# Kernel optimization log

Hardware: AMD Instinct MI355X
Metric: run time of the kernel (lower is better)

Reference implementation:

```python
import jax, jax.numpy as jnp
import numpy as np

NEG_SLOPE = 0.2


def setup_inputs() -> dict:
    key = jax.random.key(0)
    ks = jax.random.split(key, 5)
    B, N, QD, KD, H = 32, 16384, 128, 128, 128
    query = jax.random.normal(ks[0], (B, QD), dtype=jnp.float32)
    key_t = jax.random.normal(ks[1], (B, N, KD), dtype=jnp.float32)
    # nn.Linear weights: out = x @ W.T ; scale roughly like torch default init
    Wq = jax.random.normal(ks[2], (H, QD), dtype=jnp.float32) / np.sqrt(QD)
    Wk = jax.random.normal(ks[3], (H, KD), dtype=jnp.float32) / np.sqrt(KD)
    Wa = jax.random.normal(ks[4], (H,), dtype=jnp.float32) / np.sqrt(H)
    return {"query": query, "key": key_t, "Wq": Wq, "Wk": Wk, "Wa": Wa}


def reference(query, key, Wq, Wk, Wa):
    # query: [B, QD], key: [B, N, KD]
    h_query = jnp.einsum('bq,hq->bh', query, Wq)          # [B, H]
    h_key = jnp.einsum('bnk,hk->bnh', key, Wk)            # [B, N, H]
    h = h_query[:, None, :] + h_key                       # broadcast add
    e = jax.nn.leaky_relu(h, negative_slope=NEG_SLOPE)
    e = jnp.einsum('bnh,h->bn', e, Wa)                    # rank-1 attention
    e = jax.nn.softmax(e, axis=-1)                        # [B, N]
    scored = jnp.einsum('bnh,bn->bh', h_key, e)           # weighted sum over nodes
    h_prime = jax.nn.elu(scored)
    return h_prime, e
```

## Files before the change

### kernel.cpp

```cpp
#include <hip/hip_runtime.h>
#include <hip/hip_bf16.h>
#include <math.h>

#define B_ 32
#define N_ 16384
#define D_ 128
#define NEG_SLOPE 0.2f
#define CHUNKS 16
#define ITERS 16

typedef __attribute__((ext_vector_type(8))) short short8;
typedef __attribute__((ext_vector_type(4))) float f32x4;

__device__ __forceinline__ short8 cvt8(float4 x, float4 y) {
    union { unsigned u[4]; short8 s; } r;
    union { __hip_bfloat162 b; unsigned u; } t;
    t.b = __float22bfloat162_rn(make_float2(x.x, x.y)); r.u[0] = t.u;
    t.b = __float22bfloat162_rn(make_float2(x.z, x.w)); r.u[1] = t.u;
    t.b = __float22bfloat162_rn(make_float2(y.x, y.y)); r.u[2] = t.u;
    t.b = __float22bfloat162_rn(make_float2(y.z, y.w)); r.u[3] = t.u;
    return r.s;
}

template<int HALF>
__device__ __forceinline__ void compute_half(const char* lbuf, int ln, int g, int w,
                                             const short8 (&bfrag)[8][4], f32x4 (&acc)[8]) {
    const int r = w * 16 + ln;
    const unsigned swr = (unsigned)(ln & 7) << 4;
#pragma unroll
    for (int kk2 = 0; kk2 < 2; ++kk2) {
        unsigned off0 = (unsigned)(r * 256 + kk2 * 128 + g * 32);
        float4 x = *(const float4*)(lbuf + (off0 ^ swr));
        float4 y = *(const float4*)(lbuf + ((off0 + 16) ^ swr));
        short8 a = cvt8(x, y);
#pragma unroll
        for (int cf = 0; cf < 8; ++cf)
            acc[cf] = __builtin_amdgcn_mfma_f32_16x16x32_bf16(
                a, bfrag[cf][HALF * 2 + kk2], acc[cf], 0, 0, 0);
    }
}

#define WAITV(N) asm volatile("s_waitcnt vmcnt(" #N ")" ::: "memory")

__global__ __launch_bounds__(256, 2) void
main_kernel(const float* __restrict__ query, const float* __restrict__ key,
            const float* __restrict__ Wq, const float* __restrict__ Wk,
            const float* __restrict__ Wa,
            float* __restrict__ logits, float* __restrict__ part) {
    __shared__ float kbuf[4][64 * 64];
    __shared__ float comb_acc[4][D_];
    __shared__ float comb_m[4], comb_l[4];

    const int b = blockIdx.y, chunk = blockIdx.x;
    const int tid = threadIdx.x;
    const int w = tid >> 6;
    const int lane = tid & 63;
    const int ln = lane & 15;
    const int g = lane >> 4;
    const int n0 = chunk * (N_ / CHUNKS);

    short8 bfrag[8][4];
#pragma unroll
    for (int cf = 0; cf < 8; ++cf) {
        const float* wp = Wk + (size_t)(cf * 16 + ln) * D_;
#pragma unroll
        for (int kk = 0; kk < 4; ++kk) {
            const float4* p = (const float4*)(wp + kk * 32 + g * 8);
            bfrag[cf][kk] = cvt8(p[0], p[1]);
        }
    }
    float hq_r[8], wa_r[8];
    {
        const float4* qv = (const float4*)(query + (size_t)b * D_);
#pragma unroll
        for (int cf = 0; cf < 8; ++cf) {
            const float4* wv = (const float4*)(Wq + (size_t)(cf * 16 + ln) * D_ + g * 32);
            float s = 0.f;
#pragma unroll
            for (int u = 0; u < 8; ++u) {
                float4 wq = wv[u], qq = qv[g * 8 + u];
                s = fmaf(wq.x, qq.x, s); s = fmaf(wq.y, qq.y, s);
                s = fmaf(wq.z, qq.z, s); s = fmaf(wq.w, qq.w, s);
            }
            s += __shfl_xor(s, 16);
            s += __shfl_xor(s, 32);
            hq_r[cf] = s;
            wa_r[cf] = Wa[cf * 16 + ln];
        }
    }

    float m_w = -1e30f, l_w = 0.f;
    float accl[8];
#pragma unroll
    for (int cf = 0; cf < 8; ++cf) accl[cf] = 0.f;

    const char* kbase = (const char*)(key + ((size_t)b * N_ + n0) * D_);
    char* lds0 = (char*)&kbuf[0][0];

    auto stage = [&](int s) {
        const int itt = s >> 1, half = s & 1;
        const char* gt = kbase + (size_t)itt * (64 * 512) + half * 256;
        char* lb = lds0 + (s & 3) * 16384 + w * 4096;
        const int rr = lane >> 4;
        const unsigned cb = (unsigned)(lane & 15) * 16;
#pragma unroll
        for (int k = 0; k < 4; ++k) {
            int rowk = k * 4 + rr;
            unsigned src = (unsigned)((w * 16 + rowk) * 512) +
                           (cb ^ (((unsigned)(rowk & 7)) << 4));
            __builtin_amdgcn_global_load_lds(
                (const __attribute__((address_space(1))) unsigned int*)(uintptr_t)(gt + src),
                (__attribute__((address_space(3))) unsigned int*)(uintptr_t)(lb + k * 1024),
                16, 0, 0);
        }
    };

    stage(0); stage(1); stage(2);

    for (int it = 0; it < ITERS; ++it) {
        f32x4 acc[8] = {};
        {
            int s = 2 * it;
            if (s + 3 < 32) stage(s + 3);
            if (it == 0)      WAITV(12);
            else if (it < 15) WAITV(13);
            else              WAITV(6);
            compute_half<0>(lds0 + (s & 3) * 16384, ln, g, w, bfrag, acc);
        }
        {
            int s = 2 * it + 1;
            if (s + 3 < 32) stage(s + 3);
            if (it == 0)       WAITV(12);
            else if (it < 14)  WAITV(13);
            else if (it == 14) WAITV(9);
            else               WAITV(1);
            compute_half<1>(lds0 + (s & 3) * 16384, ln, g, w, bfrag, acc);
        }

        float lg[4];
#pragma unroll
        for (int j = 0; j < 4; ++j) {
            float s = 0.f;
#pragma unroll
            for (int cf = 0; cf < 8; ++cf) {
                float v = hq_r[cf] + acc[cf][j];
                v = (v > 0.f) ? v : (NEG_SLOPE * v);
                s = fmaf(v, wa_r[cf], s);
            }
            s += __shfl_xor(s, 1);
            s += __shfl_xor(s, 2);
            s += __shfl_xor(s, 4);
            s += __shfl_xor(s, 8);
            lg[j] = s;
        }
        int nbase = n0 + it * 64 + w * 16;
        if (ln == 0)
            *(float4*)&logits[(size_t)b * N_ + nbase + g * 4] =
                make_float4(lg[0], lg[1], lg[2], lg[3]);

        float mt = fmaxf(fmaxf(lg[0], lg[1]), fmaxf(lg[2], lg[3]));
        mt = fmaxf(mt, __shfl_xor(mt, 16));
        mt = fmaxf(mt, __shfl_xor(mt, 32));
        float m_new = fmaxf(m_w, mt);
        float corr = __expf(m_w - m_new);
        l_w *= corr;
#pragma unroll
        for (int cf = 0; cf < 8; ++cf) accl[cf] *= corr;
#pragma unroll
        for (int j = 0; j < 4; ++j) {
            float p = __expf(lg[j] - m_new);
            l_w += (ln == 0) ? p : 0.f;
#pragma unroll
            for (int cf = 0; cf < 8; ++cf)
                accl[cf] = fmaf(p, acc[cf][j], accl[cf]);
        }
        m_w = m_new;
    }

#pragma unroll
    for (int cf = 0; cf < 8; ++cf) {
        accl[cf] += __shfl_xor(accl[cf], 16);
        accl[cf] += __shfl_xor(accl[cf], 32);
    }
    l_w += __shfl_xor(l_w, 1);
    l_w += __shfl_xor(l_w, 2);
    l_w += __shfl_xor(l_w, 4);
    l_w += __shfl_xor(l_w, 8);
    l_w += __shfl_xor(l_w, 16);
    l_w += __shfl_xor(l_w, 32);
    if (lane < 16) {
#pragma unroll
        for (int cf = 0; cf < 8; ++cf)
            comb_acc[w][cf * 16 + ln] = accl[cf];
    }
    if (lane == 0) { comb_m[w] = m_w; comb_l[w] = l_w; }
    __syncthreads();
    if (tid < D_) {
        float mb = fmaxf(fmaxf(comb_m[0], comb_m[1]), fmaxf(comb_m[2], comb_m[3]));
        float lb = 0.f, ab = 0.f;
#pragma unroll
        for (int ww = 0; ww < 4; ++ww) {
            float cw = __expf(comb_m[ww] - mb);
            lb = fmaf(comb_l[ww], cw, lb);
            ab = fmaf(comb_acc[ww][tid], cw, ab);
        }
        float* pp = part + ((size_t)b * CHUNKS + chunk) * 132;
        pp[2 + tid] = ab;
        if (tid == 0) pp[0] = mb;
        if (tid == 1) pp[1] = lb;
    }
}

__global__ __launch_bounds__(256) void
finish_e_kernel(const float* __restrict__ part, const float* __restrict__ logits,
                float* __restrict__ out) {
    const int b = blockIdx.y, s = blockIdx.x, t = threadIdx.x;
    float mb = -1e30f;
#pragma unroll
    for (int c = 0; c < CHUNKS; ++c)
        mb = fmaxf(mb, part[((size_t)b * CHUNKS + c) * 132]);
    float lb = 0.f;
#pragma unroll
    for (int c = 0; c < CHUNKS; ++c) {
        const float* pp = part + ((size_t)b * CHUNKS + c) * 132;
        lb = fmaf(pp[1], __expf(pp[0] - mb), lb);
    }
    if (s == 0 && t < D_) {
        float ac = 0.f;
#pragma unroll
        for (int c = 0; c < CHUNKS; ++c) {
            const float* pp = part + ((size_t)b * CHUNKS + c) * 132;
            ac = fmaf(pp[2 + t], __expf(pp[0] - mb), ac);
        }
        float sc = ac / lb;
        out[b * D_ + t] = (sc > 0.f) ? sc : expm1f(sc);
    }
    float inv = 1.f / lb;
    int n4 = s * 1024 + t * 4;
    float4 lg = *(const float4*)&logits[(size_t)b * N_ + n4];
    float4 e;
    e.x = __expf(lg.x - mb) * inv;
    e.y = __expf(lg.y - mb) * inv;
    e.z = __expf(lg.z - mb) * inv;
    e.w = __expf(lg.w - mb) * inv;
    *(float4*)&out[(size_t)B_ * D_ + (size_t)b * N_ + n4] = e;
}

extern "C" void kernel_launch(void* const* d_in, const int* in_sizes, int n_in,
                              void* d_out, int out_size, void* d_ws, size_t ws_size,
                              hipStream_t stream) {
    const float* query = (const float*)d_in[0];
    const float* key   = (const float*)d_in[1];
    const float* Wq    = (const float*)d_in[2];
    const float* Wk    = (const float*)d_in[3];
    const float* Wa    = (const float*)d_in[4];
    float* out = (float*)d_out;

    float* ws     = (float*)d_ws;
    float* logits = ws;
    float* part   = logits + (size_t)B_ * N_;

    main_kernel<<<dim3(CHUNKS, B_), dim3(256), 0, stream>>>(query, key, Wq, Wk, Wa, logits, part);
    finish_e_kernel<<<dim3(16, B_), dim3(256), 0, stream>>>(part, logits, out);
}
```

Before: 79.62 us.

## Split hidden dim across warps with bf16 LDS tiles and register-staged loads

Each warp now owns 32 of the 128 hidden columns and covers all 64 rows of a tile, instead of owning 16 rows with all columns. Key tiles are loaded into registers, converted to bf16, and written to a double-buffered LDS tile, replacing the async global-to-LDS fp32 pipeline. This shrinks LDS and register use so occupancy can rise to 3 blocks per CU, and drops the conversion work inside the MFMA loop. In exchange it needs cross-warp logit reduction through LDS with two barriers per tile, and it loses the deeper async prefetch.

```diff
diff --git a/kernel.cpp b/kernel.cpp
--- a/kernel.cpp
+++ b/kernel.cpp
@@ -7,74 +7,53 @@
 #define D_ 128
 #define NEG_SLOPE 0.2f
 #define CHUNKS 16
-#define ITERS 16
+#define TILES 16
 
 typedef __attribute__((ext_vector_type(8))) short short8;
 typedef __attribute__((ext_vector_type(4))) float f32x4;
 
+__device__ __forceinline__ unsigned pk2(float lo, float hi) {
+    union { __hip_bfloat162 b; unsigned u; } t;
+    t.b = __float22bfloat162_rn(make_float2(lo, hi));
+    return t.u;
+}
 __device__ __forceinline__ short8 cvt8(float4 x, float4 y) {
     union { unsigned u[4]; short8 s; } r;
-    union { __hip_bfloat162 b; unsigned u; } t;
-    t.b = __float22bfloat162_rn(make_float2(x.x, x.y)); r.u[0] = t.u;
-    t.b = __float22bfloat162_rn(make_float2(x.z, x.w)); r.u[1] = t.u;
-    t.b = __float22bfloat162_rn(make_float2(y.x, y.y)); r.u[2] = t.u;
-    t.b = __float22bfloat162_rn(make_float2(y.z, y.w)); r.u[3] = t.u;
+    r.u[0] = pk2(x.x, x.y); r.u[1] = pk2(x.z, x.w);
+    r.u[2] = pk2(y.x, y.y); r.u[3] = pk2(y.z, y.w);
     return r.s;
 }
 
-template<int HALF>
-__device__ __forceinline__ void compute_half(const char* lbuf, int ln, int g, int w,
-                                             const short8 (&bfrag)[8][4], f32x4 (&acc)[8]) {
-    const int r = w * 16 + ln;
-    const unsigned swr = (unsigned)(ln & 7) << 4;
-#pragma unroll
-    for (int kk2 = 0; kk2 < 2; ++kk2) {
-        unsigned off0 = (unsigned)(r * 256 + kk2 * 128 + g * 32);
-        float4 x = *(const float4*)(lbuf + (off0 ^ swr));
-        float4 y = *(const float4*)(lbuf + ((off0 + 16) ^ swr));
-        short8 a = cvt8(x, y);
-#pragma unroll
-        for (int cf = 0; cf < 8; ++cf)
-            acc[cf] = __builtin_amdgcn_mfma_f32_16x16x32_bf16(
-                a, bfrag[cf][HALF * 2 + kk2], acc[cf], 0, 0, 0);
-    }
-}
-
-#define WAITV(N) asm volatile("s_waitcnt vmcnt(" #N ")" ::: "memory")
-
-__global__ __launch_bounds__(256, 2) void
+__global__ __launch_bounds__(256, 3) void
 main_kernel(const float* __restrict__ query, const float* __restrict__ key,
             const float* __restrict__ Wq, const float* __restrict__ Wk,
             const float* __restrict__ Wa,
             float* __restrict__ logits, float* __restrict__ part) {
-    __shared__ float kbuf[4][64 * 64];
-    __shared__ float comb_acc[4][D_];
-    __shared__ float comb_m[4], comb_l[4];
+    __shared__ unsigned short kt[2][64 * D_];
+    __shared__ float plds[4][64];
 
     const int b = blockIdx.y, chunk = blockIdx.x;
     const int tid = threadIdx.x;
-    const int w = tid >> 6;
-    const int lane = tid & 63;
-    const int ln = lane & 15;
-    const int g = lane >> 4;
+    const int w = tid >> 6, lane = tid & 63, ln = lane & 15, g = lane >> 4;
     const int n0 = chunk * (N_ / CHUNKS);
-
-    short8 bfrag[8][4];
-#pragma unroll
-    for (int cf = 0; cf < 8; ++cf) {
-        const float* wp = Wk + (size_t)(cf * 16 + ln) * D_;
+    const int hcol0 = w * 32 + ln;
+
+    short8 bfrag[2][4];
+#pragma unroll
+    for (int cf = 0; cf < 2; ++cf) {
+        const float* wp = Wk + (size_t)(hcol0 + cf * 16) * D_;
 #pragma unroll
         for (int kk = 0; kk < 4; ++kk) {
             const float4* p = (const float4*)(wp + kk * 32 + g * 8);
             bfrag[cf][kk] = cvt8(p[0], p[1]);
         }
     }
-    float hq_r[8], wa_r[8];
+    float hq_r[2], wa_r[2];
     {
         const float4* qv = (const float4*)(query + (size_t)b * D_);
 #pragma unroll
-        for (int cf = 0; cf < 8; ++cf) {
-            const float4* wv = (const float4*)(Wq + (size_t)(cf * 16 + ln) * D_ + g * 32);
+        for (int cf = 0; cf < 2; ++cf) {
+            const float4* wv = (const float4*)(Wq + (size_t)(hcol0 + cf * 16) * D_ + g * 32);
             float s = 0.f;
 #pragma unroll
             for (int u = 0; u < 8; ++u) {
@@ -85,130 +64,131 @@
             s += __shfl_xor(s, 16);
             s += __shfl_xor(s, 32);
             hq_r[cf] = s;
-            wa_r[cf] = Wa[cf * 16 + ln];
-        }
-    }
-
-    float m_w = -1e30f, l_w = 0.f;
-    float accl[8];
-#pragma unroll
-    for (int cf = 0; cf < 8; ++cf) accl[cf] = 0.f;
-
-    const char* kbase = (const char*)(key + ((size_t)b * N_ + n0) * D_);
-    char* lds0 = (char*)&kbuf[0][0];
-
-    auto stage = [&](int s) {
-        const int itt = s >> 1, half = s & 1;
-        const char* gt = kbase + (size_t)itt * (64 * 512) + half * 256;
-        char* lb = lds0 + (s & 3) * 16384 + w * 4096;
-        const int rr = lane >> 4;
-        const unsigned cb = (unsigned)(lane & 15) * 16;
-#pragma unroll
-        for (int k = 0; k < 4; ++k) {
-            int rowk = k * 4 + rr;
-            unsigned src = (unsigned)((w * 16 + rowk) * 512) +
-                           (cb ^ (((unsigned)(rowk & 7)) << 4));
-            __builtin_amdgcn_global_load_lds(
-                (const __attribute__((address_space(1))) unsigned int*)(uintptr_t)(gt + src),
-                (__attribute__((address_space(3))) unsigned int*)(uintptr_t)(lb + k * 1024),
-                16, 0, 0);
-        }
+            wa_r[cf] = Wa[hcol0 + cf * 16];
+        }
+    }
+
+    float m_w = -1e30f, l_w = 0.f, accl0 = 0.f, accl1 = 0.f;
+
+    const float* kbase = key + ((size_t)b * N_ + n0) * D_;
+    const int srow = w * 16 + (lane >> 2);
+    const int scol = (lane & 3) * 4;
+    float4 sregs[8];
+
+    auto issue = [&](int tt) {
+        const float* src = kbase + (size_t)(tt * 64 + srow) * D_ + scol;
+#pragma unroll
+        for (int k = 0; k < 8; ++k)
+            sregs[k] = *(const float4*)(src + k * 16);
     };
-
-    stage(0); stage(1); stage(2);
-
-    for (int it = 0; it < ITERS; ++it) {
-        f32x4 acc[8] = {};
-        {
-            int s = 2 * it;
-            if (s + 3 < 32) stage(s + 3);
-            if (it == 0)      WAITV(12);
-            else if (it < 15) WAITV(13);
-            else              WAITV(6);
-            compute_half<0>(lds0 + (s & 3) * 16384, ln, g, w, bfrag, acc);
-        }
-        {
-            int s = 2 * it + 1;
-            if (s + 3 < 32) stage(s + 3);
-            if (it == 0)       WAITV(12);
-            else if (it < 14)  WAITV(13);
-            else if (it == 14) WAITV(9);
-            else               WAITV(1);
-            compute_half<1>(lds0 + (s & 3) * 16384, ln, g, w, bfrag, acc);
-        }
-
-        float lg[4];
-#pragma unroll
-        for (int j = 0; j < 4; ++j) {
-            float s = 0.f;
-#pragma unroll
-            for (int cf = 0; cf < 8; ++cf) {
-                float v = hq_r[cf] + acc[cf][j];
-                v = (v > 0.f) ? v : (NEG_SLOPE * v);
-                s = fmaf(v, wa_r[cf], s);
-            }
-            s += __shfl_xor(s, 1);
-            s += __shfl_xor(s, 2);
-            s += __shfl_xor(s, 4);
-            s += __shfl_xor(s, 8);
-            lg[j] = s;
-        }
-        int nbase = n0 + it * 64 + w * 16;
-        if (ln == 0)
-            *(float4*)&logits[(size_t)b * N_ + nbase + g * 4] =
-                make_float4(lg[0], lg[1], lg[2], lg[3]);
-
-        float mt = fmaxf(fmaxf(lg[0], lg[1]), fmaxf(lg[2], lg[3]));
+    auto write_tile = [&](int buf) {
+        char* base = (char*)&kt[buf][0];
+#pragma unroll
+        for (int k = 0; k < 8; ++k) {
+            unsigned a = (unsigned)(srow * 256 + (lane & 3) * 8 + k * 32) ^
+                         ((unsigned)(srow & 7) << 4);
+            uint2 pk;
+            pk.x = pk2(sregs[k].x, sregs[k].y);
+            pk.y = pk2(sregs[k].z, sregs[k].w);
+            *(uint2*)(base + a) = pk;
+        }
+    };
+
+    issue(0);
+    write_tile(0);
+    issue(1);
+
+    for (int t = 0; t < TILES; ++t) {
+        if (t + 1 < TILES) {
+            write_tile((t + 1) & 1);
+            if (t + 2 < TILES) issue(t + 2);
+        }
+        asm volatile("s_waitcnt lgkmcnt(0)" ::: "memory");
+        __builtin_amdgcn_s_barrier();
+
+        f32x4 acc[4][2] = {};
+        const char* base = (const char*)&kt[t & 1][0];
+#pragma unroll
+        for (int kk = 0; kk < 4; ++kk) {
+#pragma unroll
+            for (int rf = 0; rf < 4; ++rf) {
+                int row = rf * 16 + ln;
+                short8 a = *(const short8*)(base +
+                    ((unsigned)(row * 256 + kk * 64 + g * 16) ^ ((unsigned)(row & 7) << 4)));
+                acc[rf][0] = __builtin_amdgcn_mfma_f32_16x16x32_bf16(a, bfrag[0][kk], acc[rf][0], 0, 0, 0);
+                acc[rf][1] = __builtin_amdgcn_mfma_f32_16x16x32_bf16(a, bfrag[1][kk], acc[rf][1], 0, 0, 0);
+            }
+        }
+
+#pragma unroll
+        for (int rf = 0; rf < 4; ++rf) {
+            f32x4 lp;
+#pragma unroll
+            for (int j = 0; j < 4; ++j) {
+                float v0 = hq_r[0] + acc[rf][0][j];
+                v0 = (v0 > 0.f) ? v0 : NEG_SLOPE * v0;
+                float v1 = hq_r[1] + acc[rf][1][j];
+                v1 = (v1 > 0.f) ? v1 : NEG_SLOPE * v1;
+                float s = fmaf(v0, wa_r[0], v1 * wa_r[1]);
+                s += __shfl_xor(s, 1);
+                s += __shfl_xor(s, 2);
+                s += __shfl_xor(s, 4);
+                s += __shfl_xor(s, 8);
+                lp[j] = s;
+            }
+            if (ln == 0)
+                *(f32x4*)&plds[w][rf * 16 + g * 4] = lp;
+        }
+        asm volatile("s_waitcnt lgkmcnt(0)" ::: "memory");
+        __builtin_amdgcn_s_barrier();
+
+        f32x4 p[4];
+        float mt = -1e30f;
+#pragma unroll
+        for (int rf = 0; rf < 4; ++rf) {
+            f32x4 lg = *(const f32x4*)&plds[0][rf * 16 + g * 4];
+#pragma unroll
+            for (int ww = 1; ww < 4; ++ww) {
+                f32x4 q = *(const f32x4*)&plds[ww][rf * 16 + g * 4];
+                lg[0] += q[0]; lg[1] += q[1]; lg[2] += q[2]; lg[3] += q[3];
+            }
+            p[rf] = lg;
+            mt = fmaxf(mt, fmaxf(fmaxf(lg[0], lg[1]), fmaxf(lg[2], lg[3])));
+        }
+        if (w == 3 && ln == 0) {
+            int nb = n0 + t * 64 + g * 4;
+#pragma unroll
+            for (int rf = 0; rf < 4; ++rf)
+                *(f32x4*)&logits[(size_t)b * N_ + nb + rf * 16] = p[rf];
+        }
         mt = fmaxf(mt, __shfl_xor(mt, 16));
         mt = fmaxf(mt, __shfl_xor(mt, 32));
         float m_new = fmaxf(m_w, mt);
         float corr = __expf(m_w - m_new);
-        l_w *= corr;
-#pragma unroll
-        for (int cf = 0; cf < 8; ++cf) accl[cf] *= corr;
-#pragma unroll
-        for (int j = 0; j < 4; ++j) {
-            float p = __expf(lg[j] - m_new);
-            l_w += (ln == 0) ? p : 0.f;
-#pragma unroll
-            for (int cf = 0; cf < 8; ++cf)
-                accl[cf] = fmaf(p, acc[cf][j], accl[cf]);
+        l_w *= corr; accl0 *= corr; accl1 *= corr;
+#pragma unroll
+        for (int rf = 0; rf < 4; ++rf) {
+#pragma unroll
+            for (int j = 0; j < 4; ++j) {
+                float pe = __expf(p[rf][j] - m_new);
+                l_w += pe;
+                accl0 = fmaf(pe, acc[rf][0][j], accl0);
+                accl1 = fmaf(pe, acc[rf][1][j], accl1);
+            }
         }
         m_w = m_new;
     }
 
-#pragma unroll
-    for (int cf = 0; cf < 8; ++cf) {
-        accl[cf] += __shfl_xor(accl[cf], 16);
-        accl[cf] += __shfl_xor(accl[cf], 32);
-    }
-    l_w += __shfl_xor(l_w, 1);
-    l_w += __shfl_xor(l_w, 2);
-    l_w += __shfl_xor(l_w, 4);
-    l_w += __shfl_xor(l_w, 8);
-    l_w += __shfl_xor(l_w, 16);
-    l_w += __shfl_xor(l_w, 32);
-    if (lane < 16) {
-#pragma unroll
-        for (int cf = 0; cf < 8; ++cf)
-            comb_acc[w][cf * 16 + ln] = accl[cf];
-    }
-    if (lane == 0) { comb_m[w] = m_w; comb_l[w] = l_w; }
-    __syncthreads();
-    if (tid < D_) {
-        float mb = fmaxf(fmaxf(comb_m[0], comb_m[1]), fmaxf(comb_m[2], comb_m[3]));
-        float lb = 0.f, ab = 0.f;
-#pragma unroll
-        for (int ww = 0; ww < 4; ++ww) {
-            float cw = __expf(comb_m[ww] - mb);
-            lb = fmaf(comb_l[ww], cw, lb);
-            ab = fmaf(comb_acc[ww][tid], cw, ab);
-        }
-        float* pp = part + ((size_t)b * CHUNKS + chunk) * 132;
-        pp[2 + tid] = ab;
-        if (tid == 0) pp[0] = mb;
-        if (tid == 1) pp[1] = lb;
-    }
+    l_w += __shfl_xor(l_w, 16);  l_w += __shfl_xor(l_w, 32);
+    accl0 += __shfl_xor(accl0, 16); accl0 += __shfl_xor(accl0, 32);
+    accl1 += __shfl_xor(accl1, 16); accl1 += __shfl_xor(accl1, 32);
+
+    float* pp = part + ((size_t)b * CHUNKS + chunk) * 132;
+    if (g == 0) {
+        pp[2 + w * 32 + ln] = accl0;
+        pp[2 + w * 32 + 16 + ln] = accl1;
+    }
+    if (tid == 0) { pp[0] = m_w; pp[1] = l_w; }
 }
 
 __global__ __launch_bounds__(256) void
```

Measured after the change: 85.84 us. 1.08x slower.
